# Performance work log

Hardware: AMD Instinct MI355X
Metric: run time of the kernel (lower is better)

The kernel has to match this reference:

```python
import jax, jax.numpy as jnp
import numpy as np

B, H, W, C = 64, 32, 32, 384          # batch, spatial resolution, channels
NH, WS = 12, 7                        # num_heads, window_size
HD = C // NH                          # head_dim = key_dim (attn_ratio=1)
MLP_H = 4 * C                         # mlp_ratio=4
SCALE = HD ** -0.5
EPS = 1e-5


def _bias_idxs():
    # replicate Attention.__init__ relative-position index construction
    pts = [(i, j) for i in range(WS) for j in range(WS)]
    offs, idxs = {}, []
    for p1 in pts:
        for p2 in pts:
            o = (abs(p1[0] - p2[0]), abs(p1[1] - p2[1]))
            if o not in offs:
                offs[o] = len(offs)
            idxs.append(offs[o])
    return np.array(idxs, dtype=np.int32).reshape(WS * WS, WS * WS), len(offs)


def setup_inputs() -> dict:
    key = jax.random.key(0)
    ks = jax.random.split(key, 8)
    idxs, n_off = _bias_idxs()
    s = lambda k, shape: jax.random.normal(k, shape, jnp.float32) * 0.02
    return {
        'x': jax.random.normal(ks[0], (B, H * W, C), jnp.float32),
        'ln1_g': jnp.ones((C,), jnp.float32), 'ln1_b': jnp.zeros((C,), jnp.float32),
        'qkv_w': s(ks[1], (C, 3 * C)), 'qkv_b': jnp.zeros((3 * C,), jnp.float32),
        'proj_w': s(ks[2], (C, C)), 'proj_b': jnp.zeros((C,), jnp.float32),
        'attn_biases': s(ks[3], (NH, n_off)),
        'conv_w': s(ks[4], (C, 1, 3, 3)),
        'bn_g': jnp.ones((C,), jnp.float32), 'bn_b': jnp.zeros((C,), jnp.float32),
        'bn_m': jnp.zeros((C,), jnp.float32), 'bn_v': jnp.ones((C,), jnp.float32),
        'ln2_g': jnp.ones((C,), jnp.float32), 'ln2_b': jnp.zeros((C,), jnp.float32),
        'fc1_w': s(ks[5], (C, MLP_H)), 'fc1_b': jnp.zeros((MLP_H,), jnp.float32),
        'fc2_w': s(ks[6], (MLP_H, C)), 'fc2_b': jnp.zeros((C,), jnp.float32),
        'bias_idxs': jnp.asarray(idxs),
    }


def _ln(x, g, b):
    m = x.mean(-1, keepdims=True)
    v = ((x - m) ** 2).mean(-1, keepdims=True)
    return (x - m) * jax.lax.rsqrt(v + EPS) * g + b


def _block(x, ln1_g, ln1_b, qkv_w, qkv_b, proj_w, proj_b, attn_biases,
           conv_w, bn_g, bn_b, bn_m, bn_v, ln2_g, ln2_b,
           fc1_w, fc1_b, fc2_w, fc2_b, bias_idxs):
    Bb, L, Cc = x.shape
    res = x
    # ---- window partition with padding ----
    xi = x.reshape(Bb, H, W, Cc)
    pad_b = (WS - H % WS) % WS
    pad_r = (WS - W % WS) % WS
    xi = jnp.pad(xi, ((0, 0), (0, pad_b), (0, pad_r), (0, 0)))
    pH, pW = H + pad_b, W + pad_r
    nHw, nWw = pH // WS, pW // WS
    xw = (xi.reshape(Bb, nHw, WS, nWw, WS, Cc)
            .transpose(0, 1, 3, 2, 4, 5)
            .reshape(Bb * nHw * nWw, WS * WS, Cc))
    # ---- windowed attention with gathered relative-position bias ----
    Bw, N, _ = xw.shape
    xn = _ln(xw, ln1_g, ln1_b)
    qkv = (xn @ qkv_w + qkv_b).reshape(Bw, N, NH, 3 * HD)
    q, k, v = jnp.split(qkv, 3, axis=-1)              # each [Bw, N, NH, HD]
    ab = attn_biases[:, bias_idxs]                     # gather -> [NH, N, N]
    attn = jnp.einsum('bnhd,bmhd->bhnm', q, k) * SCALE + ab
    attn = jax.nn.softmax(attn, axis=-1)
    aw = jnp.einsum('bhnm,bmhd->bnhd', attn, v).reshape(Bw, N, Cc)
    aw = aw @ proj_w + proj_b
    # ---- window merge / unpad ----
    xi = (aw.reshape(Bb, nHw, nWw, WS, WS, Cc)
            .transpose(0, 1, 3, 2, 4, 5)
            .reshape(Bb, pH, pW, Cc))[:, :H, :W]
    x = res + xi.reshape(Bb, L, Cc)
    # ---- depthwise 3x3 conv + BN (eval semantics), NCHW ----
    xc = x.transpose(0, 2, 1).reshape(Bb, Cc, H, W)
    xc = jax.lax.conv_general_dilated(xc, conv_w, (1, 1), ((1, 1), (1, 1)),
                                      feature_group_count=Cc)
    xc = ((xc - bn_m[:, None, None]) * jax.lax.rsqrt(bn_v[:, None, None] + 1e-5)
          * bn_g[:, None, None] + bn_b[:, None, None])
    x = xc.reshape(Bb, Cc, L).transpose(0, 2, 1)
    # ---- MLP (LayerNorm -> fc1 -> GELU -> fc2), residual ----
    h = jax.nn.gelu(_ln(x, ln2_g, ln2_b) @ fc1_w + fc1_b, approximate=False)
    return x + (h @ fc2_w + fc2_b)


def reference(x, ln1_g, ln1_b, qkv_w, qkv_b, proj_w, proj_b, attn_biases,
              conv_w, bn_g, bn_b, bn_m, bn_v, ln2_g, ln2_b,
              fc1_w, fc1_b, fc2_w, fc2_b, bias_idxs):
    return _block(x, ln1_g, ln1_b, qkv_w, qkv_b, proj_w, proj_b, attn_biases,
                  conv_w, bn_g, bn_b, bn_m, bn_v, ln2_g, ln2_b,
                  fc1_w, fc1_b, fc2_w, fc2_b, bias_idxs)
```

## Files before the change

kernel.cpp:

```cpp
#include <hip/hip_runtime.h>
#include <hip/hip_bf16.h>
#include <math.h>

#define NHEAD 12
#define CDIM 384
#define QKVC 1152
#define MLPH 1536
#define SCALE 0.17677669529663687f

typedef __attribute__((ext_vector_type(8))) short short8;
typedef __attribute__((ext_vector_type(4))) float f32x4;

static __device__ __forceinline__ unsigned short f2bf(float f) {
  union { __hip_bfloat16 b; unsigned short u; } c;
  c.b = __float2bfloat16(f);
  return c.u;
}

static __device__ __forceinline__ float gelu_f(float x) {
  float x3 = x * x * x;
  float y = 0.7978845608028654f * (x + 0.044715f * x3);
  float e = __expf(2.f * y);
  float th = 1.f - 2.f / (e + 1.f);
  return 0.5f * x * (1.f + th);
}

__global__ void ln_kernel(const float* __restrict__ X, const float* __restrict__ g,
                          const float* __restrict__ b, __hip_bfloat16* __restrict__ Y, int T) {
  int wid = (blockIdx.x * blockDim.x + threadIdx.x) >> 6;
  int lane = threadIdx.x & 63;
  if (wid >= T) return;
  const float* x = X + (size_t)wid * CDIM;
  float vals[6];
  float s = 0.f;
#pragma unroll
  for (int i = 0; i < 6; i++) { vals[i] = x[lane + i * 64]; s += vals[i]; }
#pragma unroll
  for (int o = 32; o > 0; o >>= 1) s += __shfl_xor(s, o);
  float m = s * (1.f / 384.f);
  float vs = 0.f;
#pragma unroll
  for (int i = 0; i < 6; i++) { float d = vals[i] - m; vs += d * d; }
#pragma unroll
  for (int o = 32; o > 0; o >>= 1) vs += __shfl_xor(vs, o);
  float rs = rsqrtf(vs * (1.f / 384.f) + 1e-5f);
  __hip_bfloat16* y = Y + (size_t)wid * CDIM;
#pragma unroll
  for (int i = 0; i < 6; i++) {
    int c = lane + i * 64;
    y[c] = __float2bfloat16((vals[i] - m) * rs * g[c] + b[c]);
  }
}

__global__ void pad_qkv_kernel(const float* __restrict__ lb, const float* __restrict__ Wq,
                               const float* __restrict__ bq, __hip_bfloat16* __restrict__ outp) {
  int j = blockIdx.x * blockDim.x + threadIdx.x;
  if (j >= QKVC) return;
  float s = bq[j];
  for (int c = 0; c < CDIM; c++) s += lb[c] * Wq[(size_t)c * QKVC + j];
  outp[j] = __float2bfloat16(s);
}

__global__ void expand_bias(const float* __restrict__ biases, const int* __restrict__ bidx,
                            float* __restrict__ Bexp, int n_off) {
  int h = blockIdx.x;
  for (int e = threadIdx.x; e < 4096; e += 256) {
    int n = e >> 6, m = e & 63;
    float v;
    if (m >= 49) v = -1e30f;
    else if (n >= 49) v = 0.f;
    else v = biases[h * n_off + bidx[n * 49 + m]];
    Bexp[h * 4096 + e] = v;
  }
}

__global__ void wt_convert(const float* __restrict__ W, __hip_bfloat16* __restrict__ Wt,
                           int K, int N) {
  __shared__ float t[32][33];
  int n0 = blockIdx.x * 32, k0 = blockIdx.y * 32;
  int tx = threadIdx.x, ty = threadIdx.y;
#pragma unroll
  for (int i = 0; i < 4; i++) t[ty + i * 8][tx] = W[(size_t)(k0 + ty + i * 8) * N + n0 + tx];
  __syncthreads();
#pragma unroll
  for (int i = 0; i < 4; i++)
    Wt[(size_t)(n0 + ty + i * 8) * K + k0 + tx] = __float2bfloat16(t[tx][ty + i * 8]);
}

__global__ void wfrag1(const float* __restrict__ W, unsigned short* __restrict__ WF) {
  int f = blockIdx.x;
  int lane = threadIdx.x;
  int wn = f & 7, kk = (f >> 3) % 12, ks = f / 96;
  int n = ks * 128 + wn * 16 + (lane & 15);
  int k = kk * 32 + (lane >> 4) * 8;
  unsigned short* dst = WF + ((size_t)f * 64 + lane) * 8;
#pragma unroll
  for (int j = 0; j < 8; j++) dst[j] = f2bf(W[(size_t)(k + j) * MLPH + n]);
}

__global__ void wfrag2(const float* __restrict__ W, unsigned short* __restrict__ WF) {
  int f = blockIdx.x;
  int lane = threadIdx.x;
  int j = f % 3, wn = (f / 3) & 7, kk = (f / 24) & 3, ks = f / 96;
  int n = wn * 48 + j * 16 + (lane & 15);
  int k = ks * 128 + kk * 32 + (lane >> 4) * 8;
  unsigned short* dst = WF + ((size_t)f * 64 + lane) * 8;
#pragma unroll
  for (int jj = 0; jj < 8; jj++) dst[jj] = f2bf(W[(size_t)(k + jj) * CDIM + n]);
}

template <int GELU, int HAS_RES, int OUT_BF16>
__global__ __launch_bounds__(256) void gemm_mfma(
    const __hip_bfloat16* __restrict__ A, const __hip_bfloat16* __restrict__ Bt,
    const float* __restrict__ bias, const float* __restrict__ res,
    void* __restrict__ Cout, int M, int N, int K) {
  __shared__ unsigned short Al[128][72];
  __shared__ unsigned short Bl[64][72];
  int tid = threadIdx.x;
  int m0 = blockIdx.y * 128, n0 = blockIdx.x * 64;
  int wave = tid >> 6, lane = tid & 63;
  int wm = (wave >> 1) * 64, wn = (wave & 1) * 32;
  int l15 = lane & 15, l4 = lane >> 4;

  int am = tid >> 1, ak = (tid & 1) * 32;
  int bn = tid >> 2, bk = (tid & 3) * 16;
  const __hip_bfloat16* Ag = A + (size_t)(m0 + am) * K + ak;
  const __hip_bfloat16* Bg = Bt + (size_t)(n0 + bn) * K + bk;

  f32x4 acc[4][2] = {};

  for (int kt = 0; kt < K; kt += 64) {
    uint4 av0 = *(const uint4*)(Ag + kt);
    uint4 av1 = *(const uint4*)(Ag + kt + 8);
    uint4 av2 = *(const uint4*)(Ag + kt + 16);
    uint4 av3 = *(const uint4*)(Ag + kt + 24);
    uint4 bv0 = *(const uint4*)(Bg + kt);
    uint4 bv1 = *(const uint4*)(Bg + kt + 8);
    __syncthreads();
    *(uint4*)&Al[am][ak]      = av0;
    *(uint4*)&Al[am][ak + 8]  = av1;
    *(uint4*)&Al[am][ak + 16] = av2;
    *(uint4*)&Al[am][ak + 24] = av3;
    *(uint4*)&Bl[bn][bk]      = bv0;
    *(uint4*)&Bl[bn][bk + 8]  = bv1;
    __syncthreads();
#pragma unroll
    for (int kk = 0; kk < 64; kk += 32) {
      short8 af[4], bfr[2];
#pragma unroll
      for (int i = 0; i < 4; i++)
        af[i] = *(const short8*)&Al[wm + i * 16 + l15][kk + l4 * 8];
#pragma unroll
      for (int j = 0; j < 2; j++)
        bfr[j] = *(const short8*)&Bl[wn + j * 16 + l15][kk + l4 * 8];
#pragma unroll
      for (int i = 0; i < 4; i++)
#pragma unroll
        for (int j = 0; j < 2; j++)
          acc[i][j] = __builtin_amdgcn_mfma_f32_16x16x32_bf16(af[i], bfr[j], acc[i][j], 0, 0, 0);
    }
  }

#pragma unroll
  for (int i = 0; i < 4; i++) {
#pragma unroll
    for (int j = 0; j < 2; j++) {
      int n = n0 + wn + j * 16 + l15;
      float bv = bias[n];
#pragma unroll
      for (int r = 0; r < 4; r++) {
        int m = m0 + wm + i * 16 + l4 * 4 + r;
        float c = acc[i][j][r] + bv;
        if (GELU) c = gelu_f(c);
        if (HAS_RES) c += res[(size_t)m * N + n];
        if (OUT_BF16)
          ((__hip_bfloat16*)Cout)[(size_t)m * N + n] = __float2bfloat16(c);
        else
          ((float*)Cout)[(size_t)m * N + n] = c;
      }
    }
  }
}

__global__ __launch_bounds__(512, 4) void mlp_fused(
    const __hip_bfloat16* __restrict__ XN, const unsigned short* __restrict__ W1F,
    const float* __restrict__ B1, const unsigned short* __restrict__ W2F,
    const float* __restrict__ B2, const float* __restrict__ X2,
    float* __restrict__ OUT) {
  __shared__ unsigned short XNl[64][388];
  __shared__ unsigned short Hl[64][132];
  int tid = threadIdx.x;
  int m0 = blockIdx.x * 64;
  int wave = tid >> 6, lane = tid & 63;
  int wn = wave;
  int l15 = lane & 15, l4 = lane >> 4;

  {
#pragma unroll
    for (int i = 0; i < 6; i++) {
      int u = tid + i * 512;
      int r = u / 48, col = (u % 48) * 8;
      *(uint4*)&XNl[r][col] =
          *(const uint4*)((const unsigned short*)XN + (size_t)(m0 + r) * 384 + col);
    }
  }

  f32x4 acc[4][3] = {};
  __syncthreads();

  for (int ks = 0; ks < 12; ks++) {
    f32x4 hacc[4] = {};
    const unsigned short* w1fb = W1F + ((size_t)(ks * 96 + wn)) * 512 + lane * 8;
#pragma unroll
    for (int kk = 0; kk < 12; kk++) {
      short8 bf0 = *(const short8*)(w1fb + kk * 4096);
#pragma unroll
      for (int i = 0; i < 4; i++) {
        short8 af = *(const short8*)&XNl[i * 16 + l15][kk * 32 + l4 * 8];
        hacc[i] = __builtin_amdgcn_mfma_f32_16x16x32_bf16(af, bf0, hacc[i], 0, 0, 0);
      }
    }
    float b1v = B1[ks * 128 + wn * 16 + l15];
    __syncthreads();
#pragma unroll
    for (int i = 0; i < 4; i++)
#pragma unroll
      for (int r = 0; r < 4; r++) {
        float c = hacc[i][r] + b1v;
        Hl[i * 16 + l4 * 4 + r][wn * 16 + l15] = f2bf(gelu_f(c));
      }
    __syncthreads();
    const unsigned short* w2fb = W2F + ((size_t)(ks * 96 + wn * 3)) * 512 + lane * 8;
#pragma unroll
    for (int kk = 0; kk < 4; kk++) {
      short8 af2[4];
#pragma unroll
      for (int i = 0; i < 4; i++)
        af2[i] = *(const short8*)&Hl[i * 16 + l15][kk * 32 + l4 * 8];
#pragma unroll
      for (int j = 0; j < 3; j++) {
        short8 bf2 = *(const short8*)(w2fb + kk * 12288 + j * 512);
#pragma unroll
        for (int i = 0; i < 4; i++)
          acc[i][j] = __builtin_amdgcn_mfma_f32_16x16x32_bf16(af2[i], bf2, acc[i][j], 0, 0, 0);
      }
    }
  }
#pragma unroll
  for (int j = 0; j < 3; j++) {
    int n = wn * 48 + j * 16 + l15;
    float bv = B2[n];
#pragma unroll
    for (int i = 0; i < 4; i++)
#pragma unroll
      for (int r = 0; r < 4; r++) {
        int m = m0 + i * 16 + l4 * 4 + r;
        OUT[(size_t)m * 384 + n] = acc[i][j][r] + bv + X2[(size_t)m * 384 + n];
      }
  }
}

__global__ __launch_bounds__(64) void attn_mfma(
    const __hip_bfloat16* __restrict__ qkv, const __hip_bfloat16* __restrict__ qkv_pad,
    const float* __restrict__ Bexp, __hip_bfloat16* __restrict__ aw) {
  int h = blockIdx.x % NHEAD;
  int w = blockIdx.x / NHEAD;
  int b = w / 25, wi = w % 25;
  int wh = wi / 5, wv = wi % 5;

  __shared__ unsigned short Q[64][40];
  __shared__ unsigned short K[64][40];
  __shared__ unsigned short Vt[32][72];
  __shared__ unsigned short P[64][72];

  int lane = threadIdx.x;
  int l15 = lane & 15, l4 = lane >> 4;

  {
    int t = lane;
    uint4 z = {0, 0, 0, 0};
    uint4 qv[4], kv[4];
    union { uint4 u[4]; unsigned short s[32]; } vu;
    bool use = t < 49;
    const unsigned short* src = (const unsigned short*)qkv_pad + h * 96;
    if (use) {
      int hh = wh * 7 + t / 7, ww = wv * 7 + t % 7;
      if (hh < 32 && ww < 32)
        src = (const unsigned short*)qkv + (size_t)(b * 1024 + hh * 32 + ww) * QKVC + h * 96;
    }
#pragma unroll
    for (int c = 0; c < 4; c++) {
      qv[c]   = use ? *(const uint4*)(src + c * 8)      : z;
      kv[c]   = use ? *(const uint4*)(src + 32 + c * 8) : z;
      vu.u[c] = use ? *(const uint4*)(src + 64 + c * 8) : z;
    }
#pragma unroll
    for (int c = 0; c < 4; c++) {
      *(uint4*)&Q[t][c * 8] = qv[c];
      *(uint4*)&K[t][c * 8] = kv[c];
    }
#pragma unroll
    for (int d = 0; d < 32; d++) Vt[d][t] = vu.s[d];
  }
  __syncthreads();

  f32x4 acc[4][4] = {};
  {
    short8 aq[4], bk[4];
#pragma unroll
    for (int i = 0; i < 4; i++) aq[i] = *(const short8*)&Q[i * 16 + l15][l4 * 8];
#pragma unroll
    for (int j = 0; j < 4; j++) bk[j] = *(const short8*)&K[j * 16 + l15][l4 * 8];
#pragma unroll
    for (int i = 0; i < 4; i++)
#pragma unroll
      for (int j = 0; j < 4; j++)
        acc[i][j] = __builtin_amdgcn_mfma_f32_16x16x32_bf16(aq[i], bk[j], acc[i][j], 0, 0, 0);
  }

  const float* Bh = Bexp + h * 4096;
  float rinv_[4][4];
#pragma unroll
  for (int i = 0; i < 4; i++) {
    float s[4][4];
#pragma unroll
    for (int j = 0; j < 4; j++)
#pragma unroll
      for (int r = 0; r < 4; r++) {
        int n = i * 16 + l4 * 4 + r, m = j * 16 + l15;
        s[j][r] = acc[i][j][r] * SCALE + Bh[n * 64 + m];
      }
#pragma unroll
    for (int r = 0; r < 4; r++) {
      float mx = fmaxf(fmaxf(s[0][r], s[1][r]), fmaxf(s[2][r], s[3][r]));
#pragma unroll
      for (int o = 1; o < 16; o <<= 1) mx = fmaxf(mx, __shfl_xor(mx, o));
      float p[4], sm = 0.f;
#pragma unroll
      for (int j = 0; j < 4; j++) { p[j] = __expf(s[j][r] - mx); sm += p[j]; }
#pragma unroll
      for (int o = 1; o < 16; o <<= 1) sm += __shfl_xor(sm, o);
      rinv_[i][r] = 1.f / sm;
      int n = i * 16 + l4 * 4 + r;
#pragma unroll
      for (int j = 0; j < 4; j++) P[n][j * 16 + l15] = f2bf(p[j]);
    }
  }
  __syncthreads();

  f32x4 o[4][2] = {};
#pragma unroll
  for (int ks = 0; ks < 2; ks++) {
    short8 pa[4], vb[2];
#pragma unroll
    for (int i = 0; i < 4; i++) pa[i] = *(const short8*)&P[i * 16 + l15][ks * 32 + l4 * 8];
#pragma unroll
    for (int j = 0; j < 2; j++) vb[j] = *(const short8*)&Vt[j * 16 + l15][ks * 32 + l4 * 8];
#pragma unroll
    for (int i = 0; i < 4; i++)
#pragma unroll
      for (int j = 0; j < 2; j++)
        o[i][j] = __builtin_amdgcn_mfma_f32_16x16x32_bf16(pa[i], vb[j], o[i][j], 0, 0, 0);
  }

#pragma unroll
  for (int i = 0; i < 4; i++)
#pragma unroll
    for (int r = 0; r < 4; r++) {
      int n = i * 16 + l4 * 4 + r;
      if (n < 49) {
        int hh = wh * 7 + n / 7, ww = wv * 7 + n % 7;
        if (hh < 32 && ww < 32) {
          __hip_bfloat16* dst = aw + (size_t)(b * 1024 + hh * 32 + ww) * CDIM + h * 32;
          float ri = rinv_[i][r];
#pragma unroll
          for (int j = 0; j < 2; j++)
            dst[j * 16 + l15] = __float2bfloat16(o[i][j][r] * ri);
        }
      }
    }
}

__global__ __launch_bounds__(384) void conv_bn_ln_kernel(
    const float* __restrict__ X, const float* __restrict__ W9,
    const float* __restrict__ g, const float* __restrict__ bb,
    const float* __restrict__ mm, const float* __restrict__ vv,
    const float* __restrict__ lg, const float* __restrict__ lb,
    float* __restrict__ X2, __hip_bfloat16* __restrict__ XN) {
  int nwg = gridDim.x;
  int id = blockIdx.x;
  int nid = (id & 7) * (nwg >> 3) + (id >> 3);
  int yh = nid & 1;
  int x = (nid >> 1) & 31;
  int b = nid >> 6;
  int c = threadIdx.x;

  float w[9];
#pragma unroll
  for (int i = 0; i < 9; i++) w[i] = W9[c * 9 + i];
  float bnsc = rsqrtf(vv[c] + 1e-5f) * g[c];
  float bnsh = bb[c] - mm[c] * bnsc;
  float lgc = lg[c], lbc = lb[c];

  bool xm = x > 0, xp = x < 31;
  const float* colbase = X + ((size_t)(b * 1024 + x)) * CDIM + c;

  __shared__ float part[2][6][2];
  int wv = threadIdx.x >> 6, ln = threadIdx.x & 63;

  float w0[3], w1[3], w2[3];
  int y0 = yh * 16;
  if (y0 == 0) {
    w0[0] = w0[1] = w0[2] = 0.f;
  } else {
    const float* p = colbase + (size_t)(y0 - 1) * 32 * CDIM;
    w0[0] = xm ? p[-CDIM] : 0.f; w0[1] = p[0]; w0[2] = xp ? p[CDIM] : 0.f;
  }
  {
    const float* p = colbase + (size_t)y0 * 32 * CDIM;
    w1[0] = xm ? p[-CDIM] : 0.f; w1[1] = p[0]; w1[2] = xp ? p[CDIM] : 0.f;
  }

  for (int y = y0; y < y0 + 16; y++) {
    if (y + 1 < 32) {
      const float* p = colbase + (size_t)(y + 1) * 32 * CDIM;
      w2[0] = xm ? p[-CDIM] : 0.f; w2[1] = p[0]; w2[2] = xp ? p[CDIM] : 0.f;
    } else {
      w2[0] = w2[1] = w2[2] = 0.f;
    }
    float acc = w0[0] * w[0] + w0[1] * w[1] + w0[2] * w[2]
              + w1[0] * w[3] + w1[1] * w[4] + w1[2] * w[5]
              + w2[0] * w[6] + w2[1] * w[7] + w2[2] * w[8];
    float r = acc * bnsc + bnsh;
    size_t tok = (size_t)(b * 1024 + y * 32 + x);
    X2[tok * CDIM + c] = r;

    float s1 = r, s2 = r * r;
#pragma unroll
    for (int o = 32; o > 0; o >>= 1) { s1 += __shfl_xor(s1, o); s2 += __shfl_xor(s2, o); }
    int pb = y & 1;
    if (ln == 0) { part[pb][wv][0] = s1; part[pb][wv][1] = s2; }
    __syncthreads();
    float ts1 = 0.f, ts2 = 0.f;
#pragma unroll
    for (int i = 0; i < 6; i++) { ts1 += part[pb][i][0]; ts2 += part[pb][i][1]; }
    float mean = ts1 * (1.f / 384.f);
    float var = ts2 * (1.f / 384.f) - mean * mean;
    float rstd = rsqrtf(var + 1e-5f);
    XN[tok * CDIM + c] = __float2bfloat16((r - mean) * rstd * lgc + lbc);

    w0[0] = w1[0]; w0[1] = w1[1]; w0[2] = w1[2];
    w1[0] = w2[0]; w1[1] = w2[1]; w1[2] = w2[2];
  }
}

extern "C" void kernel_launch(void* const* d_in, const int* in_sizes, int n_in,
                              void* d_out, int out_size, void* d_ws, size_t ws_size,
                              hipStream_t stream) {
  const float* x      = (const float*)d_in[0];
  const float* ln1_g  = (const float*)d_in[1];
  const float* ln1_b  = (const float*)d_in[2];
  const float* qkv_w  = (const float*)d_in[3];
  const float* qkv_b  = (const float*)d_in[4];
  const float* proj_w = (const float*)d_in[5];
  const float* proj_b = (const float*)d_in[6];
  const float* att_b  = (const float*)d_in[7];
  const float* conv_w = (const float*)d_in[8];
  const float* bn_g   = (const float*)d_in[9];
  const float* bn_b   = (const float*)d_in[10];
  const float* bn_m   = (const float*)d_in[11];
  const float* bn_v   = (const float*)d_in[12];
  const float* ln2_g  = (const float*)d_in[13];
  const float* ln2_b  = (const float*)d_in[14];
  const float* fc1_w  = (const float*)d_in[15];
  const float* fc1_b  = (const float*)d_in[16];
  const float* fc2_w  = (const float*)d_in[17];
  const float* fc2_b  = (const float*)d_in[18];
  const int* bias_idxs = (const int*)d_in[19];
  int n_off = in_sizes[7] / NHEAD;
  float* out = (float*)d_out;

  char* ws = (char*)d_ws;
  size_t off = 0;
  __hip_bfloat16* qkv_pad = (__hip_bfloat16*)(ws + off); off += QKVC * 2;
  off = (off + 255) & ~(size_t)255;
  float* Bexp = (float*)(ws + off); off += (size_t)NHEAD * 4096 * 4;
  __hip_bfloat16* wqkvT = (__hip_bfloat16*)(ws + off); off += (size_t)QKVC * CDIM * 2;
  __hip_bfloat16* wprojT = (__hip_bfloat16*)(ws + off); off += (size_t)CDIM * CDIM * 2;
  unsigned short* w1f = (unsigned short*)(ws + off); off += (size_t)MLPH * CDIM * 2;
  unsigned short* w2f = (unsigned short*)(ws + off); off += (size_t)CDIM * MLPH * 2;
  size_t HDR = (off + 255) & ~(size_t)255;

  const size_t PER_TOK = 5376;
  int Bc = 64;
  while (Bc > 1 && HDR + (size_t)Bc * 1024 * PER_TOK > ws_size) Bc >>= 1;
  size_t Tc = (size_t)Bc * 1024;

  off = HDR;
  __hip_bfloat16* xn = (__hip_bfloat16*)(ws + off); off += Tc * CDIM * 2;
  __hip_bfloat16* qkv = (__hip_bfloat16*)(ws + off); off += Tc * QKVC * 2;
  float* x1 = (float*)qkv;
  __hip_bfloat16* awb = (__hip_bfloat16*)(ws + off); off += Tc * CDIM * 2;
  float* x2 = (float*)(ws + off); off += Tc * CDIM * 4;

  pad_qkv_kernel<<<dim3(5), dim3(256), 0, stream>>>(ln1_b, qkv_w, qkv_b, qkv_pad);
  expand_bias<<<dim3(NHEAD), dim3(256), 0, stream>>>(att_b, bias_idxs, Bexp, n_off);
  wt_convert<<<dim3(QKVC / 32, CDIM / 32), dim3(32, 8), 0, stream>>>(qkv_w, wqkvT, CDIM, QKVC);
  wt_convert<<<dim3(CDIM / 32, CDIM / 32), dim3(32, 8), 0, stream>>>(proj_w, wprojT, CDIM, CDIM);
  wfrag1<<<dim3(1152), dim3(64), 0, stream>>>(fc1_w, w1f);
  wfrag2<<<dim3(1152), dim3(64), 0, stream>>>(fc2_w, w2f);

  for (int b0 = 0; b0 < 64; b0 += Bc) {
    const float* xa = x + (size_t)b0 * 1024 * CDIM;
    float* outa = out + (size_t)b0 * 1024 * CDIM;
    int M = (int)Tc;

    ln_kernel<<<dim3(M / 4), dim3(256), 0, stream>>>(xa, ln1_g, ln1_b, xn, M);
    gemm_mfma<0, 0, 1><<<dim3(QKVC / 64, M / 128), dim3(256), 0, stream>>>(
        xn, wqkvT, qkv_b, nullptr, qkv, M, QKVC, CDIM);
    attn_mfma<<<dim3(Bc * 25 * NHEAD), dim3(64), 0, stream>>>(qkv, qkv_pad, Bexp, awb);
    gemm_mfma<0, 1, 0><<<dim3(CDIM / 64, M / 128), dim3(256), 0, stream>>>(
        awb, wprojT, proj_b, xa, x1, M, CDIM, CDIM);
    conv_bn_ln_kernel<<<dim3(Bc * 64), dim3(384), 0, stream>>>(
        x1, conv_w, bn_g, bn_b, bn_m, bn_v, ln2_g, ln2_b, x2, xn);
    mlp_fused<<<dim3(M / 64), dim3(512), 0, stream>>>(
        xn, w1f, fc1_b, w2f, fc2_b, x2, outa);
  }
}
```

Before: 814.7 us.

## Retile fused MLP waves as 2x4 grid with register-cached A and double-buffered H

```diff
diff --git a/kernel.cpp b/kernel.cpp
--- a/kernel.cpp
+++ b/kernel.cpp
@@ -90,8 +90,8 @@
 __global__ void wfrag1(const float* __restrict__ W, unsigned short* __restrict__ WF) {
   int f = blockIdx.x;
   int lane = threadIdx.x;
-  int wn = f & 7, kk = (f >> 3) % 12, ks = f / 96;
-  int n = ks * 128 + wn * 16 + (lane & 15);
+  int g = f & 7, kk = (f >> 3) % 12, ks = f / 96;
+  int n = ks * 128 + g * 16 + (lane & 15);
   int k = kk * 32 + (lane >> 4) * 8;
   unsigned short* dst = WF + ((size_t)f * 64 + lane) * 8;
 #pragma unroll
@@ -101,8 +101,8 @@
 __global__ void wfrag2(const float* __restrict__ W, unsigned short* __restrict__ WF) {
   int f = blockIdx.x;
   int lane = threadIdx.x;
-  int j = f % 3, wn = (f / 3) & 7, kk = (f / 24) & 3, ks = f / 96;
-  int n = wn * 48 + j * 16 + (lane & 15);
+  int g2 = f % 24, kk = (f / 24) & 3, ks = f / 96;
+  int n = g2 * 16 + (lane & 15);
   int k = ks * 128 + kk * 32 + (lane >> 4) * 8;
   unsigned short* dst = WF + ((size_t)f * 64 + lane) * 8;
 #pragma unroll
@@ -182,17 +182,18 @@
   }
 }
 
-__global__ __launch_bounds__(512, 4) void mlp_fused(
+__global__ __launch_bounds__(512, 2) void mlp_fused(
     const __hip_bfloat16* __restrict__ XN, const unsigned short* __restrict__ W1F,
     const float* __restrict__ B1, const unsigned short* __restrict__ W2F,
     const float* __restrict__ B2, const float* __restrict__ X2,
     float* __restrict__ OUT) {
   __shared__ unsigned short XNl[64][388];
-  __shared__ unsigned short Hl[64][132];
+  __shared__ unsigned short Hl[2][64][132];
   int tid = threadIdx.x;
   int m0 = blockIdx.x * 64;
   int wave = tid >> 6, lane = tid & 63;
-  int wn = wave;
+  int wm = (wave >> 2) * 32;
+  int wn = wave & 3;
   int l15 = lane & 15, l4 = lane >> 4;
 
   {
@@ -204,57 +205,66 @@
           *(const uint4*)((const unsigned short*)XN + (size_t)(m0 + r) * 384 + col);
     }
   }
-
-  f32x4 acc[4][3] = {};
   __syncthreads();
 
+  short8 af[2][12];
+#pragma unroll
+  for (int i = 0; i < 2; i++)
+#pragma unroll
+    for (int kk = 0; kk < 12; kk++)
+      af[i][kk] = *(const short8*)&XNl[wm + i * 16 + l15][kk * 32 + l4 * 8];
+
+  f32x4 acc[2][6] = {};
+
   for (int ks = 0; ks < 12; ks++) {
-    f32x4 hacc[4] = {};
-    const unsigned short* w1fb = W1F + ((size_t)(ks * 96 + wn)) * 512 + lane * 8;
+    int pb = ks & 1;
+    f32x4 hacc[2][2] = {};
+    const unsigned short* w1b = W1F + ((size_t)(ks * 96 + wn * 2)) * 512 + lane * 8;
 #pragma unroll
     for (int kk = 0; kk < 12; kk++) {
-      short8 bf0 = *(const short8*)(w1fb + kk * 4096);
-#pragma unroll
-      for (int i = 0; i < 4; i++) {
-        short8 af = *(const short8*)&XNl[i * 16 + l15][kk * 32 + l4 * 8];
-        hacc[i] = __builtin_amdgcn_mfma_f32_16x16x32_bf16(af, bf0, hacc[i], 0, 0, 0);
-      }
-    }
-    float b1v = B1[ks * 128 + wn * 16 + l15];
-    __syncthreads();
-#pragma unroll
-    for (int i = 0; i < 4; i++)
-#pragma unroll
-      for (int r = 0; r < 4; r++) {
-        float c = hacc[i][r] + b1v;
-        Hl[i * 16 + l4 * 4 + r][wn * 16 + l15] = f2bf(gelu_f(c));
+      short8 bf0 = *(const short8*)(w1b + kk * 4096);
+      short8 bf1 = *(const short8*)(w1b + kk * 4096 + 512);
+      hacc[0][0] = __builtin_amdgcn_mfma_f32_16x16x32_bf16(af[0][kk], bf0, hacc[0][0], 0, 0, 0);
+      hacc[0][1] = __builtin_amdgcn_mfma_f32_16x16x32_bf16(af[0][kk], bf1, hacc[0][1], 0, 0, 0);
+      hacc[1][0] = __builtin_amdgcn_mfma_f32_16x16x32_bf16(af[1][kk], bf0, hacc[1][0], 0, 0, 0);
+      hacc[1][1] = __builtin_amdgcn_mfma_f32_16x16x32_bf16(af[1][kk], bf1, hacc[1][1], 0, 0, 0);
+    }
+    float b10 = B1[ks * 128 + wn * 32 + l15];
+    float b11 = B1[ks * 128 + wn * 32 + 16 + l15];
+#pragma unroll
+    for (int i = 0; i < 2; i++)
+#pragma unroll
+      for (int f = 0; f < 2; f++) {
+        float bv = f ? b11 : b10;
+#pragma unroll
+        for (int r = 0; r < 4; r++) {
+          float c = hacc[i][f][r] + bv;
+          Hl[pb][wm + i * 16 + l4 * 4 + r][wn * 32 + f * 16 + l15] = f2bf(gelu_f(c));
+        }
       }
     __syncthreads();
-    const unsigned short* w2fb = W2F + ((size_t)(ks * 96 + wn * 3)) * 512 + lane * 8;
+    const unsigned short* w2b = W2F + ((size_t)(ks * 96 + wn * 6)) * 512 + lane * 8;
 #pragma unroll
     for (int kk = 0; kk < 4; kk++) {
-      short8 af2[4];
-#pragma unroll
-      for (int i = 0; i < 4; i++)
-        af2[i] = *(const short8*)&Hl[i * 16 + l15][kk * 32 + l4 * 8];
-#pragma unroll
-      for (int j = 0; j < 3; j++) {
-        short8 bf2 = *(const short8*)(w2fb + kk * 12288 + j * 512);
-#pragma unroll
-        for (int i = 0; i < 4; i++)
-          acc[i][j] = __builtin_amdgcn_mfma_f32_16x16x32_bf16(af2[i], bf2, acc[i][j], 0, 0, 0);
+      short8 ha0 = *(const short8*)&Hl[pb][wm + l15][kk * 32 + l4 * 8];
+      short8 ha1 = *(const short8*)&Hl[pb][wm + 16 + l15][kk * 32 + l4 * 8];
+#pragma unroll
+      for (int j = 0; j < 6; j++) {
+        short8 bf2 = *(const short8*)(w2b + kk * 12288 + j * 512);
+        acc[0][j] = __builtin_amdgcn_mfma_f32_16x16x32_bf16(ha0, bf2, acc[0][j], 0, 0, 0);
+        acc[1][j] = __builtin_amdgcn_mfma_f32_16x16x32_bf16(ha1, bf2, acc[1][j], 0, 0, 0);
       }
     }
   }
 #pragma unroll
-  for (int j = 0; j < 3; j++) {
-    int n = wn * 48 + j * 16 + l15;
+  for (int j = 0; j < 6; j++) {
+    int n = wn * 96 + j * 16 + l15;
     float bv = B2[n];
 #pragma unroll
-    for (int i = 0; i < 4; i++)
+    for (int i = 0; i < 2; i++)
 #pragma unroll
       for (int r = 0; r < 4; r++) {
-        int m = m0 + i * 16 + l4 * 4 + r;
+        int m = m0 + wm + i * 16 + l4 * 4 + r;
         OUT[(size_t)m * 384 + n] = acc[i][j][r] + bv + X2[(size_t)m * 384 + n];
       }
   }
```

Result: slower. 1.137 ms (+39.5%).

## Split fused MLP into producer/consumer waves with double-buffered hidden tile

Applied to the files above, without the earlier changes.

```diff
diff --git a/kernel.cpp b/kernel.cpp
--- a/kernel.cpp
+++ b/kernel.cpp
@@ -90,8 +90,8 @@
 __global__ void wfrag1(const float* __restrict__ W, unsigned short* __restrict__ WF) {
   int f = blockIdx.x;
   int lane = threadIdx.x;
-  int wn = f & 7, kk = (f >> 3) % 12, ks = f / 96;
-  int n = ks * 128 + wn * 16 + (lane & 15);
+  int g = f & 7, kk = (f >> 3) % 12, ks = f / 96;
+  int n = ks * 128 + g * 16 + (lane & 15);
   int k = kk * 32 + (lane >> 4) * 8;
   unsigned short* dst = WF + ((size_t)f * 64 + lane) * 8;
 #pragma unroll
@@ -101,8 +101,8 @@
 __global__ void wfrag2(const float* __restrict__ W, unsigned short* __restrict__ WF) {
   int f = blockIdx.x;
   int lane = threadIdx.x;
-  int j = f % 3, wn = (f / 3) & 7, kk = (f / 24) & 3, ks = f / 96;
-  int n = wn * 48 + j * 16 + (lane & 15);
+  int g2 = f % 24, kk = (f / 24) & 3, ks = f / 96;
+  int n = g2 * 16 + (lane & 15);
   int k = ks * 128 + kk * 32 + (lane >> 4) * 8;
   unsigned short* dst = WF + ((size_t)f * 64 + lane) * 8;
 #pragma unroll
@@ -182,17 +182,18 @@
   }
 }
 
-__global__ __launch_bounds__(512, 4) void mlp_fused(
+__global__ __launch_bounds__(512, 2) void mlp_pc(
     const __hip_bfloat16* __restrict__ XN, const unsigned short* __restrict__ W1F,
     const float* __restrict__ B1, const unsigned short* __restrict__ W2F,
     const float* __restrict__ B2, const float* __restrict__ X2,
     float* __restrict__ OUT) {
   __shared__ unsigned short XNl[64][388];
-  __shared__ unsigned short Hl[64][132];
+  __shared__ unsigned short Hl[2][64][132];
   int tid = threadIdx.x;
   int m0 = blockIdx.x * 64;
   int wave = tid >> 6, lane = tid & 63;
-  int wn = wave;
+  int role = wave >> 2;
+  int w4 = wave & 3;
   int l15 = lane & 15, l4 = lane >> 4;
 
   {
@@ -204,59 +205,79 @@
           *(const uint4*)((const unsigned short*)XN + (size_t)(m0 + r) * 384 + col);
     }
   }
-
-  f32x4 acc[4][3] = {};
   __syncthreads();
 
-  for (int ks = 0; ks < 12; ks++) {
-    f32x4 hacc[4] = {};
-    const unsigned short* w1fb = W1F + ((size_t)(ks * 96 + wn)) * 512 + lane * 8;
-#pragma unroll
-    for (int kk = 0; kk < 12; kk++) {
-      short8 bf0 = *(const short8*)(w1fb + kk * 4096);
-#pragma unroll
-      for (int i = 0; i < 4; i++) {
-        short8 af = *(const short8*)&XNl[i * 16 + l15][kk * 32 + l4 * 8];
-        hacc[i] = __builtin_amdgcn_mfma_f32_16x16x32_bf16(af, bf0, hacc[i], 0, 0, 0);
+  f32x4 acc[4][6] = {};
+
+  for (int t = 0; t < 13; t++) {
+    if (role == 0) {
+      if (t < 12) {
+        int ks = t;
+        f32x4 hacc[4][2] = {};
+        const unsigned short* w1b = W1F + ((size_t)(ks * 96 + w4 * 2)) * 512 + lane * 8;
+#pragma unroll
+        for (int kk = 0; kk < 12; kk++) {
+          short8 bf0 = *(const short8*)(w1b + kk * 4096);
+          short8 bf1 = *(const short8*)(w1b + kk * 4096 + 512);
+#pragma unroll
+          for (int i = 0; i < 4; i++) {
+            short8 af = *(const short8*)&XNl[i * 16 + l15][kk * 32 + l4 * 8];
+            hacc[i][0] = __builtin_amdgcn_mfma_f32_16x16x32_bf16(af, bf0, hacc[i][0], 0, 0, 0);
+            hacc[i][1] = __builtin_amdgcn_mfma_f32_16x16x32_bf16(af, bf1, hacc[i][1], 0, 0, 0);
+          }
+        }
+        float b10 = B1[ks * 128 + w4 * 32 + l15];
+        float b11 = B1[ks * 128 + w4 * 32 + 16 + l15];
+        int pb = t & 1;
+#pragma unroll
+        for (int i = 0; i < 4; i++)
+#pragma unroll
+          for (int gi = 0; gi < 2; gi++) {
+            float bv = gi ? b11 : b10;
+#pragma unroll
+            for (int r = 0; r < 4; r++) {
+              float c = hacc[i][gi][r] + bv;
+              Hl[pb][i * 16 + l4 * 4 + r][w4 * 32 + gi * 16 + l15] = f2bf(gelu_f(c));
+            }
+          }
       }
-    }
-    float b1v = B1[ks * 128 + wn * 16 + l15];
+    } else {
+      if (t > 0) {
+        int ks = t - 1;
+        int pb = ks & 1;
+        const unsigned short* w2b = W2F + ((size_t)(ks * 96 + w4 * 6)) * 512 + lane * 8;
+#pragma unroll
+        for (int kk = 0; kk < 4; kk++) {
+          short8 ha[4];
+#pragma unroll
+          for (int i = 0; i < 4; i++)
+            ha[i] = *(const short8*)&Hl[pb][i * 16 + l15][kk * 32 + l4 * 8];
+#pragma unroll
+          for (int j = 0; j < 6; j++) {
+            short8 bf2 = *(const short8*)(w2b + kk * 12288 + j * 512);
+#pragma unroll
+            for (int i = 0; i < 4; i++)
+              acc[i][j] = __builtin_amdgcn_mfma_f32_16x16x32_bf16(ha[i], bf2, acc[i][j], 0, 0, 0);
+          }
+        }
+      }
+    }
     __syncthreads();
-#pragma unroll
-    for (int i = 0; i < 4; i++)
-#pragma unroll
-      for (int r = 0; r < 4; r++) {
-        float c = hacc[i][r] + b1v;
-        Hl[i * 16 + l4 * 4 + r][wn * 16 + l15] = f2bf(gelu_f(c));
-      }
-    __syncthreads();
-    const unsigned short* w2fb = W2F + ((size_t)(ks * 96 + wn * 3)) * 512 + lane * 8;
-#pragma unroll
-    for (int kk = 0; kk < 4; kk++) {
-      short8 af2[4];
+  }
+
+  if (role == 1) {
+#pragma unroll
+    for (int j = 0; j < 6; j++) {
+      int n = (w4 * 6 + j) * 16 + l15;
+      float bv = B2[n];
 #pragma unroll
       for (int i = 0; i < 4; i++)
-        af2[i] = *(const short8*)&Hl[i * 16 + l15][kk * 32 + l4 * 8];
-#pragma unroll
-      for (int j = 0; j < 3; j++) {
-        short8 bf2 = *(const short8*)(w2fb + kk * 12288 + j * 512);
-#pragma unroll
-        for (int i = 0; i < 4; i++)
-          acc[i][j] = __builtin_amdgcn_mfma_f32_16x16x32_bf16(af2[i], bf2, acc[i][j], 0, 0, 0);
-      }
-    }
-  }
-#pragma unroll
-  for (int j = 0; j < 3; j++) {
-    int n = wn * 48 + j * 16 + l15;
-    float bv = B2[n];
-#pragma unroll
-    for (int i = 0; i < 4; i++)
-#pragma unroll
-      for (int r = 0; r < 4; r++) {
-        int m = m0 + i * 16 + l4 * 4 + r;
-        OUT[(size_t)m * 384 + n] = acc[i][j][r] + bv + X2[(size_t)m * 384 + n];
-      }
+#pragma unroll
+        for (int r = 0; r < 4; r++) {
+          int m = m0 + i * 16 + l4 * 4 + r;
+          OUT[(size_t)m * 384 + n] = acc[i][j][r] + bv + X2[(size_t)m * 384 + n];
+        }
+    }
   }
 }
 
@@ -523,7 +544,7 @@
         awb, wprojT, proj_b, xa, x1, M, CDIM, CDIM);
     conv_bn_ln_kernel<<<dim3(Bc * 64), dim3(384), 0, stream>>>(
         x1, conv_w, bn_g, bn_b, bn_m, bn_v, ln2_g, ln2_b, x2, xn);
-    mlp_fused<<<dim3(M / 64), dim3(512), 0, stream>>>(
+    mlp_pc<<<dim3(M / 64), dim3(512), 0, stream>>>(
         xn, w1f, fc1_b, w2f, fc2_b, x2, outa);
   }
 }
```

After: 905.1 us. 1.11x slower.

## Fuse LayerNorm1 into QKV projection with pre-fragmented bf16 weights

Applied to the files above, without the earlier changes.

```diff
diff --git a/kernel.cpp b/kernel.cpp
--- a/kernel.cpp
+++ b/kernel.cpp
@@ -23,33 +23,6 @@
   float e = __expf(2.f * y);
   float th = 1.f - 2.f / (e + 1.f);
   return 0.5f * x * (1.f + th);
-}
-
-__global__ void ln_kernel(const float* __restrict__ X, const float* __restrict__ g,
-                          const float* __restrict__ b, __hip_bfloat16* __restrict__ Y, int T) {
-  int wid = (blockIdx.x * blockDim.x + threadIdx.x) >> 6;
-  int lane = threadIdx.x & 63;
-  if (wid >= T) return;
-  const float* x = X + (size_t)wid * CDIM;
-  float vals[6];
-  float s = 0.f;
-#pragma unroll
-  for (int i = 0; i < 6; i++) { vals[i] = x[lane + i * 64]; s += vals[i]; }
-#pragma unroll
-  for (int o = 32; o > 0; o >>= 1) s += __shfl_xor(s, o);
-  float m = s * (1.f / 384.f);
-  float vs = 0.f;
-#pragma unroll
-  for (int i = 0; i < 6; i++) { float d = vals[i] - m; vs += d * d; }
-#pragma unroll
-  for (int o = 32; o > 0; o >>= 1) vs += __shfl_xor(vs, o);
-  float rs = rsqrtf(vs * (1.f / 384.f) + 1e-5f);
-  __hip_bfloat16* y = Y + (size_t)wid * CDIM;
-#pragma unroll
-  for (int i = 0; i < 6; i++) {
-    int c = lane + i * 64;
-    y[c] = __float2bfloat16((vals[i] - m) * rs * g[c] + b[c]);
-  }
 }
 
 __global__ void pad_qkv_kernel(const float* __restrict__ lb, const float* __restrict__ Wq,
@@ -87,6 +60,17 @@
     Wt[(size_t)(n0 + ty + i * 8) * K + k0 + tx] = __float2bfloat16(t[tx][ty + i * 8]);
 }
 
+__global__ void wfragq(const float* __restrict__ W, unsigned short* __restrict__ WF) {
+  int f = blockIdx.x;
+  int lane = threadIdx.x;
+  int kk = f % 12, G = f / 12;
+  int n = G * 16 + (lane & 15);
+  int k = kk * 32 + (lane >> 4) * 8;
+  unsigned short* dst = WF + ((size_t)f * 64 + lane) * 8;
+#pragma unroll
+  for (int j = 0; j < 8; j++) dst[j] = f2bf(W[(size_t)(k + j) * QKVC + n]);
+}
+
 __global__ void wfrag1(const float* __restrict__ W, unsigned short* __restrict__ WF) {
   int f = blockIdx.x;
   int lane = threadIdx.x;
@@ -107,6 +91,65 @@
   unsigned short* dst = WF + ((size_t)f * 64 + lane) * 8;
 #pragma unroll
   for (int jj = 0; jj < 8; jj++) dst[jj] = f2bf(W[(size_t)(k + jj) * CDIM + n]);
+}
+
+__global__ __launch_bounds__(512) void ln_qkv(
+    const float* __restrict__ X, const float* __restrict__ g, const float* __restrict__ b,
+    const unsigned short* __restrict__ WQF, const float* __restrict__ BQ,
+    __hip_bfloat16* __restrict__ QKV) {
+  __shared__ unsigned short Al[64][388];
+  int tid = threadIdx.x;
+  int m0 = blockIdx.x * 64;
+  int wave = tid >> 6, lane = tid & 63;
+  int l15 = lane & 15, l4 = lane >> 4;
+
+#pragma unroll
+  for (int r8 = 0; r8 < 8; r8++) {
+    int row = wave * 8 + r8;
+    const float* xr = X + (size_t)(m0 + row) * CDIM;
+    float vals[6];
+    float s = 0.f;
+#pragma unroll
+    for (int i = 0; i < 6; i++) { vals[i] = xr[lane + i * 64]; s += vals[i]; }
+#pragma unroll
+    for (int o = 32; o > 0; o >>= 1) s += __shfl_xor(s, o);
+    float mean = s * (1.f / 384.f);
+    float vs = 0.f;
+#pragma unroll
+    for (int i = 0; i < 6; i++) { float d = vals[i] - mean; vs += d * d; }
+#pragma unroll
+    for (int o = 32; o > 0; o >>= 1) vs += __shfl_xor(vs, o);
+    float rs = rsqrtf(vs * (1.f / 384.f) + 1e-5f);
+#pragma unroll
+    for (int i = 0; i < 6; i++) {
+      int c = lane + i * 64;
+      Al[row][c] = f2bf((vals[i] - mean) * rs * g[c] + b[c]);
+    }
+  }
+  __syncthreads();
+
+  for (int rd = 0; rd < 9; rd++) {
+    int G = rd * 8 + wave;
+    f32x4 acc[4] = {};
+    const unsigned short* wb = WQF + (size_t)(G * 12) * 512 + lane * 8;
+#pragma unroll
+    for (int kk = 0; kk < 12; kk++) {
+      short8 bf = *(const short8*)(wb + kk * 512);
+#pragma unroll
+      for (int i = 0; i < 4; i++) {
+        short8 af = *(const short8*)&Al[i * 16 + l15][kk * 32 + l4 * 8];
+        acc[i] = __builtin_amdgcn_mfma_f32_16x16x32_bf16(af, bf, acc[i], 0, 0, 0);
+      }
+    }
+    int n = G * 16 + l15;
+    float bv = BQ[n];
+    __hip_bfloat16* dst = QKV + (size_t)m0 * QKVC + n;
+#pragma unroll
+    for (int i = 0; i < 4; i++)
+#pragma unroll
+      for (int r = 0; r < 4; r++)
+        dst[(size_t)(i * 16 + l4 * 4 + r) * QKVC] = __float2bfloat16(acc[i][r] + bv);
+  }
 }
 
 template <int GELU, int HAS_RES, int OUT_BF16>
@@ -485,7 +528,7 @@
   __hip_bfloat16* qkv_pad = (__hip_bfloat16*)(ws + off); off += QKVC * 2;
   off = (off + 255) & ~(size_t)255;
   float* Bexp = (float*)(ws + off); off += (size_t)NHEAD * 4096 * 4;
-  __hip_bfloat16* wqkvT = (__hip_bfloat16*)(ws + off); off += (size_t)QKVC * CDIM * 2;
+  unsigned short* wqf = (unsigned short*)(ws + off); off += (size_t)QKVC * CDIM * 2;
   __hip_bfloat16* wprojT = (__hip_bfloat16*)(ws + off); off += (size_t)CDIM * CDIM * 2;
   unsigned short* w1f = (unsigned short*)(ws + off); off += (size_t)MLPH * CDIM * 2;
   unsigned short* w2f = (unsigned short*)(ws + off); off += (size_t)CDIM * MLPH * 2;
@@ -505,7 +548,7 @@
 
   pad_qkv_kernel<<<dim3(5), dim3(256), 0, stream>>>(ln1_b, qkv_w, qkv_b, qkv_pad);
   expand_bias<<<dim3(NHEAD), dim3(256), 0, stream>>>(att_b, bias_idxs, Bexp, n_off);
-  wt_convert<<<dim3(QKVC / 32, CDIM / 32), dim3(32, 8), 0, stream>>>(qkv_w, wqkvT, CDIM, QKVC);
+  wfragq<<<dim3(864), dim3(64), 0, stream>>>(qkv_w, wqf);
   wt_convert<<<dim3(CDIM / 32, CDIM / 32), dim3(32, 8), 0, stream>>>(proj_w, wprojT, CDIM, CDIM);
   wfrag1<<<dim3(1152), dim3(64), 0, stream>>>(fc1_w, w1f);
   wfrag2<<<dim3(1152), dim3(64), 0, stream>>>(fc2_w, w2f);
@@ -515,9 +558,7 @@
     float* outa = out + (size_t)b0 * 1024 * CDIM;
     int M = (int)Tc;
 
-    ln_kernel<<<dim3(M / 4), dim3(256), 0, stream>>>(xa, ln1_g, ln1_b, xn, M);
-    gemm_mfma<0, 0, 1><<<dim3(QKVC / 64, M / 128), dim3(256), 0, stream>>>(
-        xn, wqkvT, qkv_b, nullptr, qkv, M, QKVC, CDIM);
+    ln_qkv<<<dim3(M / 64), dim3(512), 0, stream>>>(xa, ln1_g, ln1_b, wqf, qkv_b, qkv);
     attn_mfma<<<dim3(Bc * 25 * NHEAD), dim3(64), 0, stream>>>(qkv, qkv_pad, Bexp, awb);
     gemm_mfma<0, 1, 0><<<dim3(CDIM / 64, M / 128), dim3(256), 0, stream>>>(
         awb, wprojT, proj_b, xa, x1, M, CDIM, CDIM);
```

New measurement: 804.3 us. Within noise of the previous version (-1.3%).
